# Kernel tuning notes

Hardware: AMD Instinct MI355X
Metric: run time of the kernel (lower is better)

The kernel has to match this reference:

```python
import jax, jax.numpy as jnp
import numpy as np

NEG = -1000000000.0  # mask fill value used by the TF code
LEAKY_ALPHA = 0.2
TEMPERATURE = 0.5
TOP_K = 32
SHARPEN_POWER = 2.0
UNITS = 64
HEADS = 4
IN_DIM = 128
B, N = 8, 512


def sparsemax(logits):
    # Faithful port of the TF sparsemax with masked-entry handling.
    valid = (logits > -100000000.0).astype(logits.dtype)
    n_valid = jnp.maximum(jnp.sum(valid, axis=-1, keepdims=True), 1.0)
    masked = jnp.where(valid > 0, logits, 0.0)
    valid_mean = jnp.sum(masked, axis=-1, keepdims=True) / n_valid
    z = logits - valid_mean
    z = jnp.where(valid > 0, z, NEG)
    z_sorted = -jnp.sort(-z, axis=-1)  # descending
    dim = z.shape[-1]
    range_k = jnp.arange(1, dim + 1, dtype=z.dtype)
    cumsum = jnp.cumsum(z_sorted, axis=-1)
    threshold = (cumsum - 1.0) / range_k
    support = (z_sorted > threshold).astype(z.dtype)
    k_star = jnp.maximum(jnp.sum(support, axis=-1, keepdims=True), 1.0)
    tau = (jnp.sum(z_sorted * support, axis=-1, keepdims=True) - 1.0) / k_star
    return jnp.maximum(z - tau, 0.0) * valid


def setup_inputs() -> dict:
    key = jax.random.key(0)
    k1, k2, k3, k4, k5 = jax.random.split(key, 5)
    features = jax.random.normal(k1, (B, N, IN_DIM), dtype=jnp.float32)
    adjacency = jax.random.randint(k2, (B, N, N), 0, 2, dtype=jnp.int32)
    # glorot-ish scaled params
    s_w = np.sqrt(6.0 / (IN_DIM + UNITS)).astype(np.float32)
    s_a = np.sqrt(6.0 / (UNITS + 1)).astype(np.float32)
    W_src = jax.random.uniform(k3, (HEADS, IN_DIM, UNITS), jnp.float32, -s_w, s_w)
    W_dst = jax.random.uniform(k4, (HEADS, IN_DIM, UNITS), jnp.float32, -s_w, s_w)
    a = jax.random.uniform(k5, (HEADS, UNITS, 1), jnp.float32, -s_a, s_a)
    return {"features": features, "adjacency": adjacency, "W_src": W_src, "W_dst": W_dst, "a": a}


def reference(features, adjacency, W_src, W_dst, a):
    adj_f = adjacency.astype(jnp.float32)
    eye = jnp.eye(N, dtype=jnp.float32)[None]  # self loops
    mask = ((adj_f + eye) > 0)
    head_outs = []
    for h in range(HEADS):
        h_src = features @ W_src[h]          # [B,N,U]
        h_dst = features @ W_dst[h]          # [B,N,U]
        pairwise = h_src[:, :, None, :] + h_dst[:, None, :, :]   # [B,N,N,U]
        pairwise = jnp.where(pairwise > 0, pairwise, LEAKY_ALPHA * pairwise)
        scores = jnp.einsum('biju,u->bij', pairwise, a[h, :, 0])  # [B,N,N]
        scores = scores / jnp.sqrt(jnp.float32(UNITS))            # scale_scores=True
        scores = jnp.where(mask, scores, NEG)
        top_vals, _ = jax.lax.top_k(scores, TOP_K)
        kth = top_vals[:, :, -1:]
        scores = jnp.where(scores >= kth, scores, NEG)
        scores = scores / TEMPERATURE
        attn = sparsemax(scores)
        attn = jnp.power(attn + 1e-09, SHARPEN_POWER)
        attn = attn / (jnp.sum(attn, axis=-1, keepdims=True) + 1e-09)
        head_outs.append(attn @ h_src)       # [B,N,U]
    return jnp.mean(jnp.stack(head_outs, axis=-1), axis=-1)
```

## Files before the change

### kernel.cpp

```cpp
#include <hip/hip_runtime.h>
#include <hip/hip_bf16.h>

#define HEADS 4
#define UNITS 64
#define IN_DIM_ 128
#define NN 512
#define TOPK 32
#define NEGV -1e9f

__device__ __forceinline__ float readlane_f(float v, int l) {
    return __int_as_float(__builtin_amdgcn_readlane(__float_as_int(v), l));
}
__device__ __forceinline__ unsigned mapu(float x) {
    unsigned b = __float_as_uint(x);
    return b ^ ((unsigned)((int)b >> 31) | 0x80000000u);
}
__device__ __forceinline__ int mbcnt64(unsigned long long m) {
    return __builtin_amdgcn_mbcnt_hi((unsigned)(m >> 32),
           __builtin_amdgcn_mbcnt_lo((unsigned)(m & 0xFFFFFFFFull), 0u));
}

__global__ __launch_bounds__(256) void gat_k1(
    const float* __restrict__ feat, const float* __restrict__ Wsrc,
    const float* __restrict__ Wdst, const float* __restrict__ a,
    float* __restrict__ hsrc, float* __restrict__ hdstT,
    float* __restrict__ As, float* __restrict__ Ad)
{
    const int bx = blockIdx.x;
    const int rb = bx & 127;
    const int h  = (bx >> 7) & 3;
    const int sd = bx >> 9;
    const int r0 = rb * 32;
    const float* W = (sd ? Wdst : Wsrc) + h * (IN_DIM_ * UNITS);

    __shared__ float xs[32][132];
    __shared__ float ot[32][65];

    const int tid = threadIdx.x;
    #pragma unroll
    for (int it = 0; it < 4; ++it) {
        int f4 = it * 256 + tid;
        int r = f4 >> 5, c4 = (f4 & 31) << 2;
        *(float4*)&xs[r][c4] = *(const float4*)&feat[(r0 + r) * IN_DIM_ + c4];
    }
    __syncthreads();

    const int tx = tid & 15, ty = tid >> 4;
    float acc[2][4] = {{0.f,0.f,0.f,0.f},{0.f,0.f,0.f,0.f}};
    for (int k4 = 0; k4 < 128; k4 += 4) {
        float4 x0 = *(const float4*)&xs[ty*2+0][k4];
        float4 x1 = *(const float4*)&xs[ty*2+1][k4];
        float4 w0 = *(const float4*)&W[(k4+0) * UNITS + tx*4];
        float4 w1 = *(const float4*)&W[(k4+1) * UNITS + tx*4];
        float4 w2 = *(const float4*)&W[(k4+2) * UNITS + tx*4];
        float4 w3 = *(const float4*)&W[(k4+3) * UNITS + tx*4];
#define K1STEP(xc, wq) \
        acc[0][0]=fmaf(x0.xc,wq.x,acc[0][0]); acc[0][1]=fmaf(x0.xc,wq.y,acc[0][1]); \
        acc[0][2]=fmaf(x0.xc,wq.z,acc[0][2]); acc[0][3]=fmaf(x0.xc,wq.w,acc[0][3]); \
        acc[1][0]=fmaf(x1.xc,wq.x,acc[1][0]); acc[1][1]=fmaf(x1.xc,wq.y,acc[1][1]); \
        acc[1][2]=fmaf(x1.xc,wq.z,acc[1][2]); acc[1][3]=fmaf(x1.xc,wq.w,acc[1][3]);
        K1STEP(x, w0) K1STEP(y, w1) K1STEP(z, w2) K1STEP(w, w3)
#undef K1STEP
    }
    if (sd == 0) {
        #pragma unroll
        for (int r = 0; r < 2; ++r) {
            float4 v = make_float4(acc[r][0], acc[r][1], acc[r][2], acc[r][3]);
            *(float4*)&hsrc[(h * 4096 + r0 + ty*2 + r) * UNITS + tx*4] = v;
        }
    }
    #pragma unroll
    for (int r = 0; r < 2; ++r) {
        #pragma unroll
        for (int c = 0; c < 4; ++c) ot[ty*2 + r][tx*4 + c] = acc[r][c];
    }
    __syncthreads();
    if (sd == 1) {
        const int bidx = r0 >> 9, jb0 = r0 & 511;
        #pragma unroll
        for (int it = 0; it < 8; ++it) {
            int f = it * 256 + tid;
            int u = f >> 5, jl = f & 31;
            hdstT[(((h*8 + bidx) * 64 + u) << 9) + jb0 + jl] = ot[jl][u];
        }
    }
    if (tid < 32) {
        float s = 0.f;
        for (int u = 0; u < 64; ++u) s += ot[tid][u] * a[h*64 + u];
        (sd ? Ad : As)[h * 4096 + r0 + tid] = s;
    }
}

__global__ __launch_bounds__(256, 8) void gat_k2(
    const float* __restrict__ hsrc, const float* __restrict__ hdstT,
    const float* __restrict__ As_g, const float* __restrict__ Ad_g,
    const int* __restrict__ adj, const float* __restrict__ a_g,
    float* __restrict__ out)
{
    __shared__ float zAll[4 * 72];
    __shared__ int   jAll[4 * 72];

    const int tid = threadIdx.x;
    const int w = tid >> 6, lane = tid & 63;
    float* zbuf = zAll + w * 72;
    int*   jbuf = jAll + w * 72;

    const int bid = blockIdx.x;
    const int swz = (bid & 7) * 256 + (bid >> 3);
    const int wid = swz * 4 + w;
    const int slice = wid >> 8;
    const int rp    = wid & 255;
    const int h = slice >> 3, b = slice & 7;
    const int i0 = rp * 2;
    const unsigned VALIDU = mapu(-5e7f);

    const float* dbase = hdstT + (slice << 15);

    const float aqreg = 0.05f * a_g[h*64 + lane];
    const int grow0 = b*512 + i0;
    const float sreg0 = hsrc[((h*4096 + grow0) << 6) + lane];
    const float sreg1 = hsrc[((h*4096 + grow0 + 1) << 6) + lane];
    const float Asi0 = As_g[h*4096 + grow0];
    const float Asi1 = As_g[h*4096 + grow0 + 1];

    float acc0[8] = {0,0,0,0,0,0,0,0};
    float acc1[8] = {0,0,0,0,0,0,0,0};
    #pragma unroll 8
    for (int u = 0; u < 64; ++u) {
        const float4 d0 = *(const float4*)&dbase[(u << 9) + (lane << 2)];
        const float4 d1 = *(const float4*)&dbase[(u << 9) + 256 + (lane << 2)];
        const float su0 = readlane_f(sreg0, u);
        const float su1 = readlane_f(sreg1, u);
        const float qu  = readlane_f(aqreg, u);
        acc0[0]=fmaf(qu,fabsf(su0+d0.x),acc0[0]); acc0[1]=fmaf(qu,fabsf(su0+d0.y),acc0[1]);
        acc0[2]=fmaf(qu,fabsf(su0+d0.z),acc0[2]); acc0[3]=fmaf(qu,fabsf(su0+d0.w),acc0[3]);
        acc0[4]=fmaf(qu,fabsf(su0+d1.x),acc0[4]); acc0[5]=fmaf(qu,fabsf(su0+d1.y),acc0[5]);
        acc0[6]=fmaf(qu,fabsf(su0+d1.z),acc0[6]); acc0[7]=fmaf(qu,fabsf(su0+d1.w),acc0[7]);
        acc1[0]=fmaf(qu,fabsf(su1+d0.x),acc1[0]); acc1[1]=fmaf(qu,fabsf(su1+d0.y),acc1[1]);
        acc1[2]=fmaf(qu,fabsf(su1+d0.z),acc1[2]); acc1[3]=fmaf(qu,fabsf(su1+d0.w),acc1[3]);
        acc1[4]=fmaf(qu,fabsf(su1+d1.x),acc1[4]); acc1[5]=fmaf(qu,fabsf(su1+d1.y),acc1[5]);
        acc1[6]=fmaf(qu,fabsf(su1+d1.z),acc1[6]); acc1[7]=fmaf(qu,fabsf(su1+d1.w),acc1[7]);
    }
    const float4 ad0 = *(const float4*)&Ad_g[h*4096 + b*512 + (lane << 2)];
    const float4 ad1 = *(const float4*)&Ad_g[h*4096 + b*512 + 256 + (lane << 2)];

    float outAcc[2];
    for (int rr = 0; rr < 2; ++rr) {
        const int i = i0 + rr;
        const int grow = b*512 + i;
        const float Asi = rr ? Asi1 : Asi0;
        const float* accp = rr ? acc1 : acc0;
        const int4 av0 = *(const int4*)&adj[(grow << 9) + (lane << 2)];
        const int4 av1 = *(const int4*)&adj[(grow << 9) + 256 + (lane << 2)];
        const float adv[8] = {ad0.x,ad0.y,ad0.z,ad0.w,ad1.x,ad1.y,ad1.z,ad1.w};
        const int   avv[8] = {av0.x,av0.y,av0.z,av0.w,av1.x,av1.y,av1.z,av1.w};
        float m[8]; int jj[8];
        #pragma unroll
        for (int k = 0; k < 8; ++k) {
            int j = ((k >> 2) << 8) + (lane << 2) + (k & 3);
            jj[k] = j;
            float sc = accp[k] + 0.075f * (Asi + adv[k]);
            m[k] = (avv[k] > 0 || j == i) ? sc : NEGV;
        }
        unsigned ux[8];
        #pragma unroll
        for (int k = 0; k < 8; ++k) ux[k] = mapu(m[k]);
        unsigned prefix = 0u;
        for (int bit = 31; bit >= 0; --bit) {
            unsigned T = prefix | (1u << bit);
            int c0 = 0;
            #pragma unroll
            for (int k = 0; k < 8; ++k) c0 += __popcll(__ballot(ux[k] >= T));
            if (c0 >= TOPK) {
                prefix = T;
                if (c0 == TOPK) break;
            }
        }
        int cnt = 0;
        #pragma unroll
        for (int k = 0; k < 8; ++k) {
            bool sv = (ux[k] >= prefix) && (ux[k] > VALIDU);
            unsigned long long mm = __ballot(sv);
            if (sv) {
                int pos = cnt + mbcnt64(mm);
                if (pos < 64) { zbuf[pos] = 2.f * m[k]; jbuf[pos] = jj[k]; }
            }
            cnt += __popcll(mm);
        }
        if (cnt > 64) cnt = 64;
        if (lane < 4) { zbuf[cnt + lane] = -1e30f; jbuf[cnt + lane] = 0; }
        float zl = zbuf[lane];
        int   jl = jbuf[lane] & 511;
        bool act = (lane < cnt);
        if (!act) { zl = 0.f; jl = 0; }
        float tau;
        unsigned long long am = __ballot(act);
        bool cur = act;
        for (;;) {
            float s = cur ? zl : 0.f;
            #pragma unroll
            for (int d = 1; d < 64; d <<= 1) s += __shfl_xor(s, d, 64);
            const int kk = __popcll(am);
            tau = (s - 1.0f) / (float)kk;
            bool na = cur && (zl > tau);
            unsigned long long nm = __ballot(na);
            if (nm == am || nm == 0ull) break;
            am = nm; cur = na;
        }
        float wv = fmaxf(zl - tau, 0.f) + 1e-9f;
        float pl = (lane < cnt) ? wv * wv : 0.f;
        float dsum = pl;
        #pragma unroll
        for (int d = 1; d < 64; d <<= 1) dsum += __shfl_xor(dsum, d, 64);
        const float rd = 1.0f / (dsum + 1e-9f + (float)(512 - cnt) * 1e-18f);
        const float wlane = pl * rd;
        const float* hb = hsrc + ((h*4096 + b*512) << 6) + lane;
        float oa = 0.f;
        #pragma unroll
        for (int t = 0; t < TOPK; ++t) {
            float wt = readlane_f(wlane, t);
            int   jt = __builtin_amdgcn_readlane(jl, t);
            oa = fmaf(wt, hb[jt << 6], oa);
        }
        for (int t = TOPK; t < cnt; ++t) {
            float wt = readlane_f(wlane, t);
            int   jt = __builtin_amdgcn_readlane(jl, t);
            oa = fmaf(wt, hb[jt << 6], oa);
        }
        outAcc[rr] = oa;
    }
    #pragma unroll
    for (int rr = 0; rr < 2; ++rr) {
        int i = i0 + rr;
        atomicAdd(&out[((b*512 + i) << 6) + lane], 0.25f * outAcc[rr]);
    }
}

extern "C" void kernel_launch(void* const* d_in, const int* in_sizes, int n_in,
                              void* d_out, int out_size, void* d_ws, size_t ws_size,
                              hipStream_t stream) {
    const float* feat = (const float*)d_in[0];
    const int*   adj  = (const int*)d_in[1];
    const float* Wsrc = (const float*)d_in[2];
    const float* Wdst = (const float*)d_in[3];
    const float* a    = (const float*)d_in[4];
    float* out = (float*)d_out;
    float* ws  = (float*)d_ws;
    float* hsrc  = ws;
    float* hdstT = ws + 1048576;
    float* As    = ws + 2097152;
    float* Ad    = ws + 2113536;

    hipMemsetAsync(d_out, 0, (size_t)out_size * sizeof(float), stream);
    gat_k1<<<1024, 256, 0, stream>>>(feat, Wsrc, Wdst, a, hsrc, hdstT, As, Ad);
    gat_k2<<<2048, 256, 0, stream>>>(hsrc, hdstT, As, Ad, adj, a, out);
}
```

Baseline: 153.5 us.

## Interleave two-row top-k, sparsemax and gather; compute attention dot via shuffles

```diff
diff --git a/kernel.cpp b/kernel.cpp
--- a/kernel.cpp
+++ b/kernel.cpp
@@ -14,6 +14,10 @@
 __device__ __forceinline__ unsigned mapu(float x) {
     unsigned b = __float_as_uint(x);
     return b ^ ((unsigned)((int)b >> 31) | 0x80000000u);
+}
+__device__ __forceinline__ float unmapu(unsigned u) {
+    unsigned b = ((int)u < 0) ? (u ^ 0x80000000u) : ~u;
+    return __uint_as_float(b);
 }
 __device__ __forceinline__ int mbcnt64(unsigned long long m) {
     return __builtin_amdgcn_mbcnt_hi((unsigned)(m >> 32),
@@ -46,6 +50,7 @@
     __syncthreads();
 
     const int tx = tid & 15, ty = tid >> 4;
+    const float4 av = *(const float4*)&a[h*64 + tx*4];
     float acc[2][4] = {{0.f,0.f,0.f,0.f},{0.f,0.f,0.f,0.f}};
     for (int k4 = 0; k4 < 128; k4 += 4) {
         float4 x0 = *(const float4*)&xs[ty*2+0][k4];
@@ -62,20 +67,31 @@
         K1STEP(x, w0) K1STEP(y, w1) K1STEP(z, w2) K1STEP(w, w3)
 #undef K1STEP
     }
+    float p0 = acc[0][0]*av.x + acc[0][1]*av.y + acc[0][2]*av.z + acc[0][3]*av.w;
+    float p1 = acc[1][0]*av.x + acc[1][1]*av.y + acc[1][2]*av.z + acc[1][3]*av.w;
+    #pragma unroll
+    for (int d = 1; d < 16; d <<= 1) {
+        p0 += __shfl_xor(p0, d, 64);
+        p1 += __shfl_xor(p1, d, 64);
+    }
+    if (tx == 0) {
+        float* AD = sd ? Ad : As;
+        AD[h*4096 + r0 + ty*2 + 0] = p0;
+        AD[h*4096 + r0 + ty*2 + 1] = p1;
+    }
     if (sd == 0) {
         #pragma unroll
         for (int r = 0; r < 2; ++r) {
             float4 v = make_float4(acc[r][0], acc[r][1], acc[r][2], acc[r][3]);
             *(float4*)&hsrc[(h * 4096 + r0 + ty*2 + r) * UNITS + tx*4] = v;
         }
-    }
-    #pragma unroll
-    for (int r = 0; r < 2; ++r) {
-        #pragma unroll
-        for (int c = 0; c < 4; ++c) ot[ty*2 + r][tx*4 + c] = acc[r][c];
-    }
-    __syncthreads();
-    if (sd == 1) {
+    } else {
+        #pragma unroll
+        for (int r = 0; r < 2; ++r) {
+            #pragma unroll
+            for (int c = 0; c < 4; ++c) ot[ty*2 + r][tx*4 + c] = acc[r][c];
+        }
+        __syncthreads();
         const int bidx = r0 >> 9, jb0 = r0 & 511;
         #pragma unroll
         for (int it = 0; it < 8; ++it) {
@@ -83,11 +99,6 @@
             int u = f >> 5, jl = f & 31;
             hdstT[(((h*8 + bidx) * 64 + u) << 9) + jb0 + jl] = ot[jl][u];
         }
-    }
-    if (tid < 32) {
-        float s = 0.f;
-        for (int u = 0; u < 64; ++u) s += ot[tid][u] * a[h*64 + u];
-        (sd ? Ad : As)[h * 4096 + r0 + tid] = s;
     }
 }
 
@@ -97,13 +108,13 @@
     const int* __restrict__ adj, const float* __restrict__ a_g,
     float* __restrict__ out)
 {
-    __shared__ float zAll[4 * 72];
-    __shared__ int   jAll[4 * 72];
+    __shared__ float zAll[4][2][64];
+    __shared__ int   jAll[4][2][64];
 
     const int tid = threadIdx.x;
     const int w = tid >> 6, lane = tid & 63;
-    float* zbuf = zAll + w * 72;
-    int*   jbuf = jAll + w * 72;
+    float* z0 = zAll[w][0]; float* z1 = zAll[w][1];
+    int*   j0 = jAll[w][0]; int*   j1 = jAll[w][1];
 
     const int bid = blockIdx.x;
     const int swz = (bid & 7) * 256 + (bid >> 3);
@@ -143,97 +154,124 @@
     }
     const float4 ad0 = *(const float4*)&Ad_g[h*4096 + b*512 + (lane << 2)];
     const float4 ad1 = *(const float4*)&Ad_g[h*4096 + b*512 + 256 + (lane << 2)];
-
-    float outAcc[2];
-    for (int rr = 0; rr < 2; ++rr) {
-        const int i = i0 + rr;
-        const int grow = b*512 + i;
-        const float Asi = rr ? Asi1 : Asi0;
-        const float* accp = rr ? acc1 : acc0;
-        const int4 av0 = *(const int4*)&adj[(grow << 9) + (lane << 2)];
-        const int4 av1 = *(const int4*)&adj[(grow << 9) + 256 + (lane << 2)];
-        const float adv[8] = {ad0.x,ad0.y,ad0.z,ad0.w,ad1.x,ad1.y,ad1.z,ad1.w};
-        const int   avv[8] = {av0.x,av0.y,av0.z,av0.w,av1.x,av1.y,av1.z,av1.w};
-        float m[8]; int jj[8];
+    const int4 av0 = *(const int4*)&adj[(grow0 << 9) + (lane << 2)];
+    const int4 av1 = *(const int4*)&adj[(grow0 << 9) + 256 + (lane << 2)];
+    const int4 bv0 = *(const int4*)&adj[((grow0 + 1) << 9) + (lane << 2)];
+    const int4 bv1 = *(const int4*)&adj[((grow0 + 1) << 9) + 256 + (lane << 2)];
+
+    unsigned ux0[8], ux1[8];
+    {
+        const float advk[8] = {ad0.x,ad0.y,ad0.z,ad0.w,ad1.x,ad1.y,ad1.z,ad1.w};
+        const int   a0k[8]  = {av0.x,av0.y,av0.z,av0.w,av1.x,av1.y,av1.z,av1.w};
+        const int   a1k[8]  = {bv0.x,bv0.y,bv0.z,bv0.w,bv1.x,bv1.y,bv1.z,bv1.w};
         #pragma unroll
         for (int k = 0; k < 8; ++k) {
             int j = ((k >> 2) << 8) + (lane << 2) + (k & 3);
-            jj[k] = j;
-            float sc = accp[k] + 0.075f * (Asi + adv[k]);
-            m[k] = (avv[k] > 0 || j == i) ? sc : NEGV;
-        }
-        unsigned ux[8];
-        #pragma unroll
-        for (int k = 0; k < 8; ++k) ux[k] = mapu(m[k]);
-        unsigned prefix = 0u;
-        for (int bit = 31; bit >= 0; --bit) {
-            unsigned T = prefix | (1u << bit);
-            int c0 = 0;
-            #pragma unroll
-            for (int k = 0; k < 8; ++k) c0 += __popcll(__ballot(ux[k] >= T));
-            if (c0 >= TOPK) {
-                prefix = T;
-                if (c0 == TOPK) break;
+            float s0 = acc0[k] + 0.075f * (Asi0 + advk[k]);
+            float s1 = acc1[k] + 0.075f * (Asi1 + advk[k]);
+            ux0[k] = mapu((a0k[k] > 0 || j == i0)     ? s0 : NEGV);
+            ux1[k] = mapu((a1k[k] > 0 || j == i0 + 1) ? s1 : NEGV);
+        }
+    }
+    unsigned p0 = 0u, p1 = 0u;
+    bool done0 = false, done1 = false;
+    for (int bit = 31; bit >= 0 && !(done0 && done1); --bit) {
+        if (!done0) {
+            unsigned T = p0 | (1u << bit);
+            int c = 0;
+            #pragma unroll
+            for (int k = 0; k < 8; ++k) c += __popcll(__ballot(ux0[k] >= T));
+            if (c >= TOPK) { p0 = T; if (c == TOPK) done0 = true; }
+        }
+        if (!done1) {
+            unsigned T = p1 | (1u << bit);
+            int c = 0;
+            #pragma unroll
+            for (int k = 0; k < 8; ++k) c += __popcll(__ballot(ux1[k] >= T));
+            if (c >= TOPK) { p1 = T; if (c == TOPK) done1 = true; }
+        }
+    }
+    int cnt0 = 0, cnt1 = 0;
+    #pragma unroll
+    for (int k = 0; k < 8; ++k) {
+        int j = ((k >> 2) << 8) + (lane << 2) + (k & 3);
+        bool s0 = (ux0[k] >= p0) && (ux0[k] > VALIDU);
+        bool s1 = (ux1[k] >= p1) && (ux1[k] > VALIDU);
+        unsigned long long m0 = __ballot(s0);
+        unsigned long long m1 = __ballot(s1);
+        if (s0) { int pos = cnt0 + mbcnt64(m0); if (pos < 64) { z0[pos] = 2.f * unmapu(ux0[k]); j0[pos] = j; } }
+        if (s1) { int pos = cnt1 + mbcnt64(m1); if (pos < 64) { z1[pos] = 2.f * unmapu(ux1[k]); j1[pos] = j; } }
+        cnt0 += __popcll(m0); cnt1 += __popcll(m1);
+    }
+    if (cnt0 > 64) cnt0 = 64;
+    if (cnt1 > 64) cnt1 = 64;
+    float zl0 = z0[lane], zl1 = z1[lane];
+    int   jl0 = j0[lane] & 511, jl1 = j1[lane] & 511;
+    bool act0 = lane < cnt0, act1 = lane < cnt1;
+    if (!act0) { zl0 = 0.f; jl0 = 0; }
+    if (!act1) { zl1 = 0.f; jl1 = 0; }
+    float tau0 = 0.f, tau1 = 0.f;
+    {
+        unsigned long long am0 = __ballot(act0), am1 = __ballot(act1);
+        bool cur0 = act0, cur1 = act1;
+        bool cv0 = false, cv1 = false;
+        for (int it = 0; it < 64 && !(cv0 && cv1); ++it) {
+            float s0 = cur0 ? zl0 : 0.f;
+            float s1 = cur1 ? zl1 : 0.f;
+            #pragma unroll
+            for (int d = 1; d < 64; d <<= 1) {
+                s0 += __shfl_xor(s0, d, 64);
+                s1 += __shfl_xor(s1, d, 64);
             }
-        }
-        int cnt = 0;
-        #pragma unroll
-        for (int k = 0; k < 8; ++k) {
-            bool sv = (ux[k] >= prefix) && (ux[k] > VALIDU);
-            unsigned long long mm = __ballot(sv);
-            if (sv) {
-                int pos = cnt + mbcnt64(mm);
-                if (pos < 64) { zbuf[pos] = 2.f * m[k]; jbuf[pos] = jj[k]; }
+            if (!cv0) {
+                tau0 = (s0 - 1.0f) / (float)__popcll(am0);
+                bool na = cur0 && (zl0 > tau0);
+                unsigned long long nm = __ballot(na);
+                if (nm == am0 || nm == 0ull) cv0 = true; else { am0 = nm; cur0 = na; }
             }
-            cnt += __popcll(mm);
-        }
-        if (cnt > 64) cnt = 64;
-        if (lane < 4) { zbuf[cnt + lane] = -1e30f; jbuf[cnt + lane] = 0; }
-        float zl = zbuf[lane];
-        int   jl = jbuf[lane] & 511;
-        bool act = (lane < cnt);
-        if (!act) { zl = 0.f; jl = 0; }
-        float tau;
-        unsigned long long am = __ballot(act);
-        bool cur = act;
-        for (;;) {
-            float s = cur ? zl : 0.f;
-            #pragma unroll
-            for (int d = 1; d < 64; d <<= 1) s += __shfl_xor(s, d, 64);
-            const int kk = __popcll(am);
-            tau = (s - 1.0f) / (float)kk;
-            bool na = cur && (zl > tau);
-            unsigned long long nm = __ballot(na);
-            if (nm == am || nm == 0ull) break;
-            am = nm; cur = na;
-        }
-        float wv = fmaxf(zl - tau, 0.f) + 1e-9f;
-        float pl = (lane < cnt) ? wv * wv : 0.f;
-        float dsum = pl;
-        #pragma unroll
-        for (int d = 1; d < 64; d <<= 1) dsum += __shfl_xor(dsum, d, 64);
-        const float rd = 1.0f / (dsum + 1e-9f + (float)(512 - cnt) * 1e-18f);
-        const float wlane = pl * rd;
-        const float* hb = hsrc + ((h*4096 + b*512) << 6) + lane;
-        float oa = 0.f;
-        #pragma unroll
-        for (int t = 0; t < TOPK; ++t) {
-            float wt = readlane_f(wlane, t);
-            int   jt = __builtin_amdgcn_readlane(jl, t);
-            oa = fmaf(wt, hb[jt << 6], oa);
-        }
-        for (int t = TOPK; t < cnt; ++t) {
-            float wt = readlane_f(wlane, t);
-            int   jt = __builtin_amdgcn_readlane(jl, t);
-            oa = fmaf(wt, hb[jt << 6], oa);
-        }
-        outAcc[rr] = oa;
-    }
-    #pragma unroll
-    for (int rr = 0; rr < 2; ++rr) {
-        int i = i0 + rr;
-        atomicAdd(&out[((b*512 + i) << 6) + lane], 0.25f * outAcc[rr]);
-    }
+            if (!cv1) {
+                tau1 = (s1 - 1.0f) / (float)__popcll(am1);
+                bool na = cur1 && (zl1 > tau1);
+                unsigned long long nm = __ballot(na);
+                if (nm == am1 || nm == 0ull) cv1 = true; else { am1 = nm; cur1 = na; }
+            }
+        }
+    }
+    float wv0 = fmaxf(zl0 - tau0, 0.f) + 1e-9f;
+    float wv1 = fmaxf(zl1 - tau1, 0.f) + 1e-9f;
+    float pl0 = act0 ? wv0 * wv0 : 0.f;
+    float pl1 = act1 ? wv1 * wv1 : 0.f;
+    float ds0 = pl0, ds1 = pl1;
+    #pragma unroll
+    for (int d = 1; d < 64; d <<= 1) {
+        ds0 += __shfl_xor(ds0, d, 64);
+        ds1 += __shfl_xor(ds1, d, 64);
+    }
+    const float w0l = pl0 * (1.0f / (ds0 + 1e-9f + (float)(512 - cnt0) * 1e-18f));
+    const float w1l = pl1 * (1.0f / (ds1 + 1e-9f + (float)(512 - cnt1) * 1e-18f));
+    const float* hb = hsrc + ((h*4096 + b*512) << 6) + lane;
+    float oa0 = 0.f, oa1 = 0.f;
+    #pragma unroll
+    for (int t = 0; t < TOPK; ++t) {
+        float wt0 = readlane_f(w0l, t);
+        float wt1 = readlane_f(w1l, t);
+        int   jt0 = __builtin_amdgcn_readlane(jl0, t);
+        int   jt1 = __builtin_amdgcn_readlane(jl1, t);
+        oa0 = fmaf(wt0, hb[jt0 << 6], oa0);
+        oa1 = fmaf(wt1, hb[jt1 << 6], oa1);
+    }
+    for (int t = TOPK; t < cnt0; ++t) {
+        float wt = readlane_f(w0l, t);
+        int   jt = __builtin_amdgcn_readlane(jl0, t);
+        oa0 = fmaf(wt, hb[jt << 6], oa0);
+    }
+    for (int t = TOPK; t < cnt1; ++t) {
+        float wt = readlane_f(w1l, t);
+        int   jt = __builtin_amdgcn_readlane(jl1, t);
+        oa1 = fmaf(wt, hb[jt << 6], oa1);
+    }
+    atomicAdd(&out[((b*512 + i0)     << 6) + lane], 0.25f * oa0);
+    atomicAdd(&out[((b*512 + i0 + 1) << 6) + lane], 0.25f * oa1);
 }
 
 extern "C" void kernel_launch(void* const* d_in, const int* in_sizes, int n_in,
```

Measured after the change: 152.9 us. About the same (-0.4%).
